# Kernel tuning notes

Hardware: AMD Instinct MI355X
Metric: run time of the kernel (lower is better)

The kernel has to match this reference:

```python
import jax, jax.numpy as jnp
import numpy as np

B, T, D, E, H, K = 4, 4096, 1024, 8, 512, 2  # batch, seq, n_embed, num_experts, bottleneck, top_k


def setup_inputs() -> dict:
    key = jax.random.key(0)
    ks = jax.random.split(key, 8)
    s = 0.02  # param scale (original zero-inits adapters; random used for a meaningful baseline)
    return {
        "x": jax.random.normal(ks[0], (B, T, D), jnp.float32),
        "Wr": (jax.random.normal(ks[1], (D, E), jnp.float32) * s),
        "br": jnp.zeros((E,), jnp.float32),
        "Wn": (jax.random.normal(ks[2], (D, E), jnp.float32) * s),
        "bn": jnp.zeros((E,), jnp.float32),
        "Wd": (jax.random.normal(ks[3], (E, D, H), jnp.float32) * s),
        "bd": jnp.zeros((E, H), jnp.float32),
        "Wu": (jax.random.normal(ks[4], (E, H, D), jnp.float32) * s),
        "bu": jnp.zeros((E, D), jnp.float32),
        "noise": jax.random.normal(ks[5], (B, T, E), jnp.float32),
        "top_k": K,
    }


def reference(x, Wr, br, Wn, bn, Wd, bd, Wu, bu, noise, top_k):
    # --- NoisyTopkRouter ---
    logits = x @ Wr + br                                   # [B,T,E]
    noise_logits = x @ Wn + bn                             # [B,T,E]
    noisy = logits + noise * jax.nn.softplus(noise_logits)  # randn * softplus(noise_logits)
    _, idx = jax.lax.top_k(noisy, top_k)                   # [B,T,K]
    # mask of selected experts; where(mask, noisy, -inf) == scatter(top_k_logits into -inf)
    mask = jax.nn.one_hot(idx, noisy.shape[-1], dtype=jnp.bool_).any(axis=-2)  # [B,T,E]
    sparse = jnp.where(mask, noisy, -jnp.inf)
    gates = jax.nn.softmax(sparse, axis=-1)                # zeros for unselected experts

    # --- Experts (dense grouped form; gate==0 exactly kills unselected experts incl. biases) ---
    down = jnp.einsum('btd,edh->bteh', x, Wd) + bd         # [B,T,E,H]
    hidden = jax.nn.gelu(down, approximate=False)          # torch GELU is exact (erf)
    up = jnp.einsum('bteh,ehd->bted', hidden, Wu) + bu     # [B,T,E,D]
    return jnp.einsum('bted,bte->btd', up, gates)          # gate-weighted combine
```

## Files before the change

### kernel.cpp

```cpp
#include <hip/hip_runtime.h>
#include <hip/hip_bf16.h>
#include <hip/hip_fp16.h>
#include <math.h>

#define DD   1024
#define EE   8
#define HH   512
#define NTOK 16384
#define NG   16
#define MAXMT 24

typedef __attribute__((ext_vector_type(8))) short short8;
typedef __attribute__((ext_vector_type(4))) float floatx4;

__device__ __forceinline__ ushort f2bfu(float f) {
    __hip_bfloat16 h = __float2bfloat16(f);
    return *reinterpret_cast<ushort*>(&h);
}

__device__ __forceinline__ void glds16(const void* g, void* l) {
    __builtin_amdgcn_global_load_lds(
        (const __attribute__((address_space(1))) unsigned int*)g,
        (__attribute__((address_space(3))) unsigned int*)l, 16, 0, 0);
}

__global__ void zero_k(int* __restrict__ cnt) {
    if (blockIdx.x == 0 && threadIdx.x < 256) cnt[threadIdx.x] = 0;
}

__global__ __launch_bounds__(256) void trans_k(const float* __restrict__ src, ushort* __restrict__ dst,
                                               const int R, const int C) {
    const int e = blockIdx.z, r0 = blockIdx.y * 64, c0 = blockIdx.x * 64;
    __shared__ float t[64][65];
    const int tid = threadIdx.x;
    const int cseg = (tid & 15) * 4, rr = tid >> 4;
#pragma unroll
    for (int j = 0; j < 4; ++j) {
        const int r = rr + j * 16;
        const float4 v = *(const float4*)(src + ((size_t)e * R + r0 + r) * C + c0 + cseg);
        t[r][cseg] = v.x; t[r][cseg+1] = v.y; t[r][cseg+2] = v.z; t[r][cseg+3] = v.w;
    }
    __syncthreads();
    const int rseg = (tid & 15) * 4;
#pragma unroll
    for (int j = 0; j < 4; ++j) {
        const int crow = (tid >> 4) + j * 16;
        ushort o[4];
#pragma unroll
        for (int q = 0; q < 4; ++q) o[q] = f2bfu(t[rseg + q][crow]);
        *(uint2*)(dst + ((size_t)e * C + c0 + crow) * R + r0 + rseg) = *(uint2*)o;
    }
}

__global__ __launch_bounds__(256) void router_k(
    const float* __restrict__ x, const float* __restrict__ Wr, const float* __restrict__ br,
    const float* __restrict__ Wn, const float* __restrict__ bn, const float* __restrict__ noise,
    int* __restrict__ cnt, unsigned* __restrict__ entries, ushort* __restrict__ xb)
{
    const int wave = threadIdx.x >> 6;
    const int lane = threadIdx.x & 63;
    const int t = blockIdx.x * 4 + wave;

    float accr[EE], accn[EE];
#pragma unroll
    for (int e = 0; e < EE; ++e) { accr[e] = 0.f; accn[e] = 0.f; }

    const float* xr = x + (size_t)t * DD;
    ushort* xbr = xb + (size_t)t * DD;
#pragma unroll 4
    for (int it = 0; it < DD / 64; ++it) {
        const int d = it * 64 + lane;
        const float xv = xr[d];
        xbr[d] = f2bfu(xv);
        float wr[8], wn[8];
        *(float4*)&wr[0] = *(const float4*)(Wr + (size_t)d * EE);
        *(float4*)&wr[4] = *(const float4*)(Wr + (size_t)d * EE + 4);
        *(float4*)&wn[0] = *(const float4*)(Wn + (size_t)d * EE);
        *(float4*)&wn[4] = *(const float4*)(Wn + (size_t)d * EE + 4);
#pragma unroll
        for (int e = 0; e < EE; ++e) {
            accr[e] = fmaf(xv, wr[e], accr[e]);
            accn[e] = fmaf(xv, wn[e], accn[e]);
        }
    }
#pragma unroll
    for (int off = 32; off > 0; off >>= 1) {
#pragma unroll
        for (int e = 0; e < EE; ++e) {
            accr[e] += __shfl_xor(accr[e], off);
            accn[e] += __shfl_xor(accn[e], off);
        }
    }
    if (lane == 0) {
        float noisy[EE];
#pragma unroll
        for (int e = 0; e < EE; ++e) {
            const float lg = accr[e] + br[e];
            const float nl = accn[e] + bn[e];
            const float sp = fmaxf(nl, 0.f) + log1pf(expf(-fabsf(nl)));
            noisy[e] = lg + noise[(size_t)t * EE + e] * sp;
        }
        int i0 = 0;
#pragma unroll
        for (int e = 1; e < EE; ++e) if (noisy[e] > noisy[i0]) i0 = e;
        int i1 = (i0 == 0) ? 1 : 0;
#pragma unroll
        for (int e = 0; e < EE; ++e) if (e != i0 && noisy[e] > noisy[i1]) i1 = e;
        const float ex = expf(noisy[i1] - noisy[i0]);
        const float g0 = 1.f / (1.f + ex);
        const float g1 = ex / (1.f + ex);
        __half h0 = __float2half_rn(g0), h1 = __float2half_rn(g1);
        const unsigned u0 = (unsigned)t | ((unsigned)*reinterpret_cast<ushort*>(&h0) << 16);
        const unsigned u1 = (unsigned)t | ((unsigned)*reinterpret_cast<ushort*>(&h1) << 16);
        const int ga = i0 * 2 + 0, gb = i1 * 2 + 1;
        int p0 = atomicAdd(&cnt[ga * 16], 1);
        entries[ga * NTOK + p0] = u0;
        int p1 = atomicAdd(&cnt[gb * 16], 1);
        entries[gb * NTOK + p1] = u1;
    }
}

__global__ void offsets_k(const int* __restrict__ cnt, int* __restrict__ off) {
    if (threadIdx.x == 0 && blockIdx.x == 0) {
        int s = 0;
        for (int g = 0; g < NG; ++g) { off[g] = s; s += cnt[g * 16]; }
    }
}


__global__ __launch_bounds__(256) void down_k(
    const ushort* __restrict__ xb, const ushort* __restrict__ WdT, const float* __restrict__ bd,
    const int* __restrict__ cnt, const int* __restrict__ off,
    const unsigned* __restrict__ entries, ushort* __restrict__ hid)
{
    const int g = blockIdx.z, e = g >> 1;
    const int n_g = cnt[g * 16];
    const int tm = blockIdx.y;
    if (tm * 128 >= n_g) return;
    const int n0 = blockIdx.x * 128;

    __shared__ __align__(16) ushort As[128 * 64];
    __shared__ __align__(16) ushort Bs[128 * 64];
    __shared__ unsigned ecache[128];

    const int tid = threadIdx.x, lane = tid & 63, w = tid >> 6;
    const int wm = w >> 1, wn = w & 1;
    const int fr = lane & 15, fq = lane >> 4;

    if (tid < 128) {
        const int ridx = min(tm * 128 + tid, n_g - 1);
        ecache[tid] = entries[g * NTOK + ridx];
    }
    __syncthreads();

    const int lr = lane >> 3, seg = lane & 7;
    const int slog = seg ^ lr;
    const ushort* gA[4]; const ushort* gB[4];
    char* lA[4]; char* lB[4];
    const ushort* WTe = WdT + (size_t)e * HH * DD;
#pragma unroll
    for (int j = 0; j < 4; ++j) {
        const int row = w * 32 + j * 8 + lr;
        const int tok = (int)(ecache[row] & 0xFFFFu);
        gA[j] = xb + (size_t)tok * DD + slog * 8;
        gB[j] = WTe + (size_t)(n0 + row) * DD + slog * 8;
        lA[j] = (char*)As + (size_t)(w * 256 + j * 64) * 16;
        lB[j] = (char*)Bs + (size_t)(w * 256 + j * 64) * 16;
    }

    floatx4 acc[4][4];
#pragma unroll
    for (int i = 0; i < 4; ++i)
#pragma unroll
        for (int j = 0; j < 4; ++j) acc[i][j] = (floatx4){0.f, 0.f, 0.f, 0.f};

    const int axr = wm * 64 + fr;
    const int bxr = wn * 64 + fr;

    for (int k0 = 0; k0 < DD; k0 += 64) {
        __syncthreads();
#pragma unroll
        for (int j = 0; j < 4; ++j) { glds16(gA[j] + k0, lA[j]); glds16(gB[j] + k0, lB[j]); }
        __syncthreads();
#pragma unroll
        for (int kh = 0; kh < 2; ++kh) {
            short8 a[4], b[4];
#pragma unroll
            for (int mt = 0; mt < 4; ++mt) {
                const int r = axr + mt * 16;
                a[mt] = *(const short8*)&As[r * 64 + ((kh * 4 + fq) ^ (r & 7)) * 8];
            }
#pragma unroll
            for (int nt = 0; nt < 4; ++nt) {
                const int r = bxr + nt * 16;
                b[nt] = *(const short8*)&Bs[r * 64 + ((kh * 4 + fq) ^ (r & 7)) * 8];
            }
#pragma unroll
            for (int mt = 0; mt < 4; ++mt)
#pragma unroll
                for (int nt = 0; nt < 4; ++nt)
                    acc[mt][nt] = __builtin_amdgcn_mfma_f32_16x16x32_bf16(a[mt], b[nt], acc[mt][nt], 0, 0, 0);
        }
    }

    const int hbase = off[g] + tm * 128;
#pragma unroll
    for (int nt = 0; nt < 4; ++nt) {
        const int n = n0 + wn * 64 + nt * 16 + fr;
        const float bias = bd[e * HH + n];
#pragma unroll
        for (int mt = 0; mt < 4; ++mt)
#pragma unroll
            for (int i = 0; i < 4; ++i) {
                const int rl = wm * 64 + mt * 16 + fq * 4 + i;
                if (tm * 128 + rl < n_g) {
                    const float v = acc[mt][nt][i] + bias;
                    const float ge = 0.5f * v * (1.f + erff(v * 0.7071067811865475f));
                    hid[(size_t)(hbase + rl) * HH + n] = f2bfu(ge);
                }
            }
    }
}

__global__ __launch_bounds__(256) void up_k(
    const ushort* __restrict__ hid, const ushort* __restrict__ WuT, const float* __restrict__ bu,
    const int* __restrict__ cnt, const int* __restrict__ off,
    const unsigned* __restrict__ entries, float* __restrict__ out)
{
    const int g = blockIdx.z, e = g >> 1;
    const int n_g = cnt[g * 16];
    const int tm = blockIdx.y;
    if (tm * 128 >= n_g) return;
    const int n0 = blockIdx.x * 128;

    __shared__ __align__(16) ushort As[128 * 64];
    __shared__ __align__(16) ushort Bs[128 * 64];
    __shared__ unsigned ecache[128];

    const int tid = threadIdx.x, lane = tid & 63, w = tid >> 6;
    const int wm = w >> 1, wn = w & 1;
    const int fr = lane & 15, fq = lane >> 4;

    if (tid < 128) {
        const int ridx = min(tm * 128 + tid, n_g - 1);
        ecache[tid] = entries[g * NTOK + ridx];
    }
    __syncthreads();

    const int lr = lane >> 3, seg = lane & 7;
    const int slog = seg ^ lr;
    const ushort* gA[4]; const ushort* gB[4];
    char* lA[4]; char* lB[4];
    const ushort* WTe = WuT + (size_t)e * DD * HH;
    const int hbase = off[g];
#pragma unroll
    for (int j = 0; j < 4; ++j) {
        const int row = w * 32 + j * 8 + lr;
        const int ar = min(tm * 128 + row, n_g - 1);
        gA[j] = hid + (size_t)(hbase + ar) * HH + slog * 8;
        gB[j] = WTe + (size_t)(n0 + row) * HH + slog * 8;
        lA[j] = (char*)As + (size_t)(w * 256 + j * 64) * 16;
        lB[j] = (char*)Bs + (size_t)(w * 256 + j * 64) * 16;
    }

    floatx4 acc[4][4];
#pragma unroll
    for (int i = 0; i < 4; ++i)
#pragma unroll
        for (int j = 0; j < 4; ++j) acc[i][j] = (floatx4){0.f, 0.f, 0.f, 0.f};

    const int axr = wm * 64 + fr;
    const int bxr = wn * 64 + fr;

    for (int k0 = 0; k0 < HH; k0 += 64) {
        __syncthreads();
#pragma unroll
        for (int j = 0; j < 4; ++j) { glds16(gA[j] + k0, lA[j]); glds16(gB[j] + k0, lB[j]); }
        __syncthreads();
#pragma unroll
        for (int kh = 0; kh < 2; ++kh) {
            short8 a[4], b[4];
#pragma unroll
            for (int mt = 0; mt < 4; ++mt) {
                const int r = axr + mt * 16;
                a[mt] = *(const short8*)&As[r * 64 + ((kh * 4 + fq) ^ (r & 7)) * 8];
            }
#pragma unroll
            for (int nt = 0; nt < 4; ++nt) {
                const int r = bxr + nt * 16;
                b[nt] = *(const short8*)&Bs[r * 64 + ((kh * 4 + fq) ^ (r & 7)) * 8];
            }
#pragma unroll
            for (int mt = 0; mt < 4; ++mt)
#pragma unroll
                for (int nt = 0; nt < 4; ++nt)
                    acc[mt][nt] = __builtin_amdgcn_mfma_f32_16x16x32_bf16(a[mt], b[nt], acc[mt][nt], 0, 0, 0);
        }
    }

#pragma unroll
    for (int nt = 0; nt < 4; ++nt) {
        const int n = n0 + wn * 64 + nt * 16 + fr;
        const float bias = bu[e * DD + n];
#pragma unroll
        for (int mt = 0; mt < 4; ++mt)
#pragma unroll
            for (int i = 0; i < 4; ++i) {
                const int rl = wm * 64 + mt * 16 + fq * 4 + i;
                if (tm * 128 + rl < n_g) {
                    const unsigned en = ecache[rl];
                    const int tok = (int)(en & 0xFFFFu);
                    ushort hb = (ushort)(en >> 16);
                    const float gate = __half2float(*reinterpret_cast<__half*>(&hb));
                    unsafeAtomicAdd(out + (size_t)tok * DD + n, (acc[mt][nt][i] + bias) * gate);
                }
            }
    }
}

extern "C" void kernel_launch(void* const* d_in, const int* in_sizes, int n_in,
                              void* d_out, int out_size, void* d_ws, size_t ws_size,
                              hipStream_t stream)
{
    const float* x     = (const float*)d_in[0];
    const float* Wr    = (const float*)d_in[1];
    const float* br    = (const float*)d_in[2];
    const float* Wn    = (const float*)d_in[3];
    const float* bn    = (const float*)d_in[4];
    const float* Wd    = (const float*)d_in[5];
    const float* bd    = (const float*)d_in[6];
    const float* Wu    = (const float*)d_in[7];
    const float* bu    = (const float*)d_in[8];
    const float* noise = (const float*)d_in[9];

    char* ws = (char*)d_ws;
    int*      cnt     = (int*)(ws + 0);
    int*      off     = (int*)(ws + 1024);
    unsigned* entries = (unsigned*)(ws + 2048);
    ushort*   xb      = (ushort*)(ws + 1050624);
    ushort*   WdT     = (ushort*)(ws + 34605056);
    ushort*   WuT     = (ushort*)(ws + 42993664);
    ushort*   hid     = (ushort*)(ws + 51382272);

    hipMemsetAsync(d_out, 0, (size_t)NTOK * DD * sizeof(float), stream);
    zero_k<<<1, 256, 0, stream>>>(cnt);
    trans_k<<<dim3(HH / 64, DD / 64, EE), 256, 0, stream>>>(Wd, WdT, DD, HH);
    trans_k<<<dim3(DD / 64, HH / 64, EE), 256, 0, stream>>>(Wu, WuT, HH, DD);
    router_k<<<NTOK / 4, 256, 0, stream>>>(x, Wr, br, Wn, bn, noise, cnt, entries, xb);
    offsets_k<<<1, 64, 0, stream>>>(cnt, off);
    down_k<<<dim3(HH / 128, MAXMT, NG), 256, 0, stream>>>(xb, WdT, bd, cnt, off, entries, hid);
    up_k<<<dim3(DD / 128, MAXMT, NG), 256, 0, stream>>>(hid, WuT, bu, cnt, off, entries, (float*)d_out);
}
```

Measured before the change: 497.4 us.

## Batch router over four tokens per wave and replace output atomics with two-pass writes

The router now has each wave handle four tokens, so every Wr/Wn weight load is reused across four tokens and the grid shrinks fourfold. The up-projection is split into two launches by top-k slot. Slot 0 stores directly to the output and slot 1 does a plain read-modify-write, which removes the output memset and the float atomic adds. This relies on each token appearing exactly once per slot group, and it serializes the up-projection into two launches with smaller grids.

```diff
diff --git a/kernel.cpp b/kernel.cpp
--- a/kernel.cpp
+++ b/kernel.cpp
@@ -59,64 +59,72 @@
 {
     const int wave = threadIdx.x >> 6;
     const int lane = threadIdx.x & 63;
-    const int t = blockIdx.x * 4 + wave;
-
-    float accr[EE], accn[EE];
-#pragma unroll
-    for (int e = 0; e < EE; ++e) { accr[e] = 0.f; accn[e] = 0.f; }
-
-    const float* xr = x + (size_t)t * DD;
-    ushort* xbr = xb + (size_t)t * DD;
-#pragma unroll 4
+    const int t0 = (blockIdx.x * 4 + wave) * 4;
+
+    float accr[EE * 4], accn[EE * 4];
+#pragma unroll
+    for (int i = 0; i < EE * 4; ++i) { accr[i] = 0.f; accn[i] = 0.f; }
+
+#pragma unroll 2
     for (int it = 0; it < DD / 64; ++it) {
         const int d = it * 64 + lane;
-        const float xv = xr[d];
-        xbr[d] = f2bfu(xv);
         float wr[8], wn[8];
         *(float4*)&wr[0] = *(const float4*)(Wr + (size_t)d * EE);
         *(float4*)&wr[4] = *(const float4*)(Wr + (size_t)d * EE + 4);
         *(float4*)&wn[0] = *(const float4*)(Wn + (size_t)d * EE);
         *(float4*)&wn[4] = *(const float4*)(Wn + (size_t)d * EE + 4);
-#pragma unroll
-        for (int e = 0; e < EE; ++e) {
-            accr[e] = fmaf(xv, wr[e], accr[e]);
-            accn[e] = fmaf(xv, wn[e], accn[e]);
-        }
+        float xv[4];
+#pragma unroll
+        for (int tk = 0; tk < 4; ++tk) {
+            xv[tk] = x[(size_t)(t0 + tk) * DD + d];
+            xb[(size_t)(t0 + tk) * DD + d] = f2bfu(xv[tk]);
+        }
+#pragma unroll
+        for (int e = 0; e < EE; ++e)
+#pragma unroll
+            for (int tk = 0; tk < 4; ++tk) {
+                accr[e * 4 + tk] = fmaf(xv[tk], wr[e], accr[e * 4 + tk]);
+                accn[e * 4 + tk] = fmaf(xv[tk], wn[e], accn[e * 4 + tk]);
+            }
     }
 #pragma unroll
     for (int off = 32; off > 0; off >>= 1) {
 #pragma unroll
-        for (int e = 0; e < EE; ++e) {
-            accr[e] += __shfl_xor(accr[e], off);
-            accn[e] += __shfl_xor(accn[e], off);
+        for (int i = 0; i < EE * 4; ++i) {
+            accr[i] += __shfl_xor(accr[i], off);
+            accn[i] += __shfl_xor(accn[i], off);
         }
     }
     if (lane == 0) {
-        float noisy[EE];
-#pragma unroll
-        for (int e = 0; e < EE; ++e) {
-            const float lg = accr[e] + br[e];
-            const float nl = accn[e] + bn[e];
-            const float sp = fmaxf(nl, 0.f) + log1pf(expf(-fabsf(nl)));
-            noisy[e] = lg + noise[(size_t)t * EE + e] * sp;
-        }
-        int i0 = 0;
-#pragma unroll
-        for (int e = 1; e < EE; ++e) if (noisy[e] > noisy[i0]) i0 = e;
-        int i1 = (i0 == 0) ? 1 : 0;
-#pragma unroll
-        for (int e = 0; e < EE; ++e) if (e != i0 && noisy[e] > noisy[i1]) i1 = e;
-        const float ex = expf(noisy[i1] - noisy[i0]);
-        const float g0 = 1.f / (1.f + ex);
-        const float g1 = ex / (1.f + ex);
-        __half h0 = __float2half_rn(g0), h1 = __float2half_rn(g1);
-        const unsigned u0 = (unsigned)t | ((unsigned)*reinterpret_cast<ushort*>(&h0) << 16);
-        const unsigned u1 = (unsigned)t | ((unsigned)*reinterpret_cast<ushort*>(&h1) << 16);
-        const int ga = i0 * 2 + 0, gb = i1 * 2 + 1;
-        int p0 = atomicAdd(&cnt[ga * 16], 1);
-        entries[ga * NTOK + p0] = u0;
-        int p1 = atomicAdd(&cnt[gb * 16], 1);
-        entries[gb * NTOK + p1] = u1;
+#pragma unroll
+        for (int tk = 0; tk < 4; ++tk) {
+            const int t = t0 + tk;
+            float noisy[EE];
+#pragma unroll
+            for (int e = 0; e < EE; ++e) {
+                const float lg = accr[e * 4 + tk] + br[e];
+                const float nl = accn[e * 4 + tk] + bn[e];
+                const float sp = fmaxf(nl, 0.f) + log1pf(expf(-fabsf(nl)));
+                noisy[e] = lg + noise[(size_t)t * EE + e] * sp;
+            }
+            int i0 = 0;
+#pragma unroll
+            for (int e = 1; e < EE; ++e) if (noisy[e] > noisy[i0]) i0 = e;
+            int i1 = (i0 == 0) ? 1 : 0;
+#pragma unroll
+            for (int e = 0; e < EE; ++e) if (e != i0 && noisy[e] > noisy[i1]) i1 = e;
+            const float ex = expf(noisy[i1] - noisy[i0]);
+            const float g0 = 1.f / (1.f + ex);
+            const float g1 = ex / (1.f + ex);
+            __half h0 = __float2half_rn(g0), h1 = __float2half_rn(g1);
+            const unsigned u0 = (unsigned)t | ((unsigned)*reinterpret_cast<ushort*>(&h0) << 16);
+            const unsigned u1 = (unsigned)t | ((unsigned)*reinterpret_cast<ushort*>(&h1) << 16);
+            const int ga = i0 * 2 + 0, gb = i1 * 2 + 1;
+            int p0 = atomicAdd(&cnt[ga * 16], 1);
+            entries[ga * NTOK + p0] = u0;
+            int p1 = atomicAdd(&cnt[gb * 16], 1);
+            entries[gb * NTOK + p1] = u1;
+        }
     }
 }
 
@@ -225,9 +233,9 @@
 __global__ __launch_bounds__(256) void up_k(
     const ushort* __restrict__ hid, const ushort* __restrict__ WuT, const float* __restrict__ bu,
     const int* __restrict__ cnt, const int* __restrict__ off,
-    const unsigned* __restrict__ entries, float* __restrict__ out)
+    const unsigned* __restrict__ entries, float* __restrict__ out, const int s)
 {
-    const int g = blockIdx.z, e = g >> 1;
+    const int e = blockIdx.z, g = e * 2 + s;
     const int n_g = cnt[g * 16];
     const int tm = blockIdx.y;
     if (tm * 128 >= n_g) return;
@@ -312,7 +320,10 @@
                     const int tok = (int)(en & 0xFFFFu);
                     ushort hb = (ushort)(en >> 16);
                     const float gate = __half2float(*reinterpret_cast<__half*>(&hb));
-                    unsafeAtomicAdd(out + (size_t)tok * DD + n, (acc[mt][nt][i] + bias) * gate);
+                    const float v = (acc[mt][nt][i] + bias) * gate;
+                    float* op = out + (size_t)tok * DD + n;
+                    if (s == 0) *op = v;
+                    else        *op += v;
                 }
             }
     }
@@ -342,12 +353,12 @@
     ushort*   WuT     = (ushort*)(ws + 42993664);
     ushort*   hid     = (ushort*)(ws + 51382272);
 
-    hipMemsetAsync(d_out, 0, (size_t)NTOK * DD * sizeof(float), stream);
     zero_k<<<1, 256, 0, stream>>>(cnt);
     trans_k<<<dim3(HH / 64, DD / 64, EE), 256, 0, stream>>>(Wd, WdT, DD, HH);
     trans_k<<<dim3(DD / 64, HH / 64, EE), 256, 0, stream>>>(Wu, WuT, HH, DD);
-    router_k<<<NTOK / 4, 256, 0, stream>>>(x, Wr, br, Wn, bn, noise, cnt, entries, xb);
+    router_k<<<NTOK / 16, 256, 0, stream>>>(x, Wr, br, Wn, bn, noise, cnt, entries, xb);
     offsets_k<<<1, 64, 0, stream>>>(cnt, off);
     down_k<<<dim3(HH / 128, MAXMT, NG), 256, 0, stream>>>(xb, WdT, bd, cnt, off, entries, hid);
-    up_k<<<dim3(DD / 128, MAXMT, NG), 256, 0, stream>>>(hid, WuT, bu, cnt, off, entries, (float*)d_out);
-}
+    up_k<<<dim3(DD / 128, MAXMT, EE), 256, 0, stream>>>(hid, WuT, bu, cnt, off, entries, (float*)d_out, 0);
+    up_k<<<dim3(DD / 128, MAXMT, EE), 256, 0, stream>>>(hid, WuT, bu, cnt, off, entries, (float*)d_out, 1);
+}
```

Result: no change. 504.2 us (+1.4%).

## Replace atomic scatter-add with per-slot bf16 writes and a combine kernel

Applied to the files above, without the earlier changes.

The up-projection no longer atomically adds gated expert outputs into a pre-zeroed fp32 output. It now writes each token's contribution as bf16 into one of two slots, chosen by the top-k group parity, and a new combine kernel sums the two slots into the output. This removes the output memset and the global atomics. The down and up grids are also flattened to 1D with the N-tile index varying fastest, so blocks sharing an A row-tile run close together. The cost is extra slot traffic and an extra launch, plus precision loss from rounding each expert's contribution to bf16 before summing.

```diff
diff --git a/kernel.cpp b/kernel.cpp
--- a/kernel.cpp
+++ b/kernel.cpp
@@ -16,6 +16,9 @@
 __device__ __forceinline__ ushort f2bfu(float f) {
     __hip_bfloat16 h = __float2bfloat16(f);
     return *reinterpret_cast<ushort*>(&h);
+}
+__device__ __forceinline__ float bfu2f(ushort u) {
+    union { unsigned u; float f; } cv; cv.u = ((unsigned)u) << 16; return cv.f;
 }
 
 __device__ __forceinline__ void glds16(const void* g, void* l) {
@@ -133,11 +136,13 @@
     const int* __restrict__ cnt, const int* __restrict__ off,
     const unsigned* __restrict__ entries, ushort* __restrict__ hid)
 {
-    const int g = blockIdx.z, e = g >> 1;
+    const int bx = blockIdx.x;
+    const int n0 = (bx & 3) * 128;
+    const int tmg = bx >> 2;
+    const int tm = tmg % MAXMT;
+    const int g = tmg / MAXMT, e = g >> 1;
     const int n_g = cnt[g * 16];
-    const int tm = blockIdx.y;
     if (tm * 128 >= n_g) return;
-    const int n0 = blockIdx.x * 128;
 
     __shared__ __align__(16) ushort As[128 * 64];
     __shared__ __align__(16) ushort Bs[128 * 64];
@@ -225,13 +230,15 @@
 __global__ __launch_bounds__(256) void up_k(
     const ushort* __restrict__ hid, const ushort* __restrict__ WuT, const float* __restrict__ bu,
     const int* __restrict__ cnt, const int* __restrict__ off,
-    const unsigned* __restrict__ entries, float* __restrict__ out)
-{
-    const int g = blockIdx.z, e = g >> 1;
+    const unsigned* __restrict__ entries, ushort* __restrict__ slots)
+{
+    const int bx = blockIdx.x;
+    const int n0 = (bx & 7) * 128;
+    const int tmg = bx >> 3;
+    const int tm = tmg % MAXMT;
+    const int g = tmg / MAXMT, e = g >> 1, slot = g & 1;
     const int n_g = cnt[g * 16];
-    const int tm = blockIdx.y;
     if (tm * 128 >= n_g) return;
-    const int n0 = blockIdx.x * 128;
 
     __shared__ __align__(16) ushort As[128 * 64];
     __shared__ __align__(16) ushort Bs[128 * 64];
@@ -312,10 +319,27 @@
                     const int tok = (int)(en & 0xFFFFu);
                     ushort hb = (ushort)(en >> 16);
                     const float gate = __half2float(*reinterpret_cast<__half*>(&hb));
-                    unsafeAtomicAdd(out + (size_t)tok * DD + n, (acc[mt][nt][i] + bias) * gate);
+                    const float v = (acc[mt][nt][i] + bias) * gate;
+                    slots[((size_t)tok * 2 + slot) * DD + n] = f2bfu(v);
                 }
             }
     }
+}
+
+__global__ __launch_bounds__(256) void combine_k(
+    const ushort* __restrict__ slots, float* __restrict__ out)
+{
+    const size_t flat = ((size_t)blockIdx.x * 256 + threadIdx.x) * 8;
+    const size_t t = flat >> 10;
+    const size_t d = flat & (DD - 1);
+    union { uint4 v; ushort h[8]; } a, b;
+    a.v = *(const uint4*)(slots + ((t * 2 + 0) << 10) + d);
+    b.v = *(const uint4*)(slots + ((t * 2 + 1) << 10) + d);
+    float o[8];
+#pragma unroll
+    for (int j = 0; j < 8; ++j) o[j] = bfu2f(a.h[j]) + bfu2f(b.h[j]);
+    *(float4*)(out + flat) = *(const float4*)&o[0];
+    *(float4*)(out + flat + 4) = *(const float4*)&o[4];
 }
 
 extern "C" void kernel_launch(void* const* d_in, const int* in_sizes, int n_in,
@@ -341,13 +365,14 @@
     ushort*   WdT     = (ushort*)(ws + 34605056);
     ushort*   WuT     = (ushort*)(ws + 42993664);
     ushort*   hid     = (ushort*)(ws + 51382272);
-
-    hipMemsetAsync(d_out, 0, (size_t)NTOK * DD * sizeof(float), stream);
+    ushort*   slots   = (ushort*)(ws + 84936704);
+
     zero_k<<<1, 256, 0, stream>>>(cnt);
     trans_k<<<dim3(HH / 64, DD / 64, EE), 256, 0, stream>>>(Wd, WdT, DD, HH);
     trans_k<<<dim3(DD / 64, HH / 64, EE), 256, 0, stream>>>(Wu, WuT, HH, DD);
     router_k<<<NTOK / 4, 256, 0, stream>>>(x, Wr, br, Wn, bn, noise, cnt, entries, xb);
     offsets_k<<<1, 64, 0, stream>>>(cnt, off);
-    down_k<<<dim3(HH / 128, MAXMT, NG), 256, 0, stream>>>(xb, WdT, bd, cnt, off, entries, hid);
-    up_k<<<dim3(DD / 128, MAXMT, NG), 256, 0, stream>>>(hid, WuT, bu, cnt, off, entries, (float*)d_out);
-}
+    down_k<<<NG * MAXMT * 4, 256, 0, stream>>>(xb, WdT, bd, cnt, off, entries, hid);
+    up_k<<<NG * MAXMT * 8, 256, 0, stream>>>(hid, WuT, bu, cnt, off, entries, slots);
+    combine_k<<<(NTOK * DD) / (256 * 8), 256, 0, stream>>>(slots, (float*)d_out);
+}
```

Result: faster. 446.2 us (-10.3%).
